# Kernel optimization log

Hardware: AMD Instinct MI355X
Metric: run time of the kernel (lower is better)

Reference implementation:

```python
import jax, jax.numpy as jnp
import numpy as np

NUM_HEADS = 16

def _rope_tables(seq_len, dim, dtype):
    # LongLlamaRotaryEmbedding: inv_freq = 1/10000^(2i/d), emb = cat(freqs, freqs)
    inv_freq = 1.0 / (10000.0 ** (jnp.arange(0, dim, 2, dtype=jnp.float32) / dim))
    t = jnp.arange(seq_len, dtype=jnp.float32)
    freqs = t[:, None] * inv_freq[None, :]            # [S, D/2]
    emb = jnp.concatenate([freqs, freqs], axis=-1)    # [S, D]
    return jnp.cos(emb).astype(dtype), jnp.sin(emb).astype(dtype)

def _rotate_half(x):
    x1, x2 = jnp.split(x, 2, axis=-1)
    return jnp.concatenate([-x2, x1], axis=-1)

def _rotate_one(x, cos, sin, pos):
    # x: [B,H,S,D]; pos: [B,S] int -> gather-indexed RoPE
    c = cos[pos][:, None, :, :]  # [B,1,S,D]
    s = sin[pos][:, None, :, :]
    return x * c + _rotate_half(x) * s

def setup_inputs() -> dict:
    key = jax.random.key(0)
    B, S, HID = 1, 4096, 2048
    ks = jax.random.split(key, 5)
    hidden_states = jax.random.normal(ks[0], (B, S, HID), dtype=jnp.float32)
    # causal additive mask [B,1,S,S]: 0 where allowed, large negative above diagonal
    causal = jnp.tril(jnp.ones((S, S), dtype=bool))
    attention_mask = jnp.where(causal, 0.0, -1e9).astype(jnp.float32)[None, None]
    attention_mask = jnp.broadcast_to(attention_mask, (B, 1, S, S))
    position_ids = jnp.broadcast_to(jnp.arange(S, dtype=jnp.int64), (B, S))
    scale = 0.02
    Wq = jax.random.normal(ks[1], (HID, HID), dtype=jnp.float32) * scale
    Wk = jax.random.normal(ks[2], (HID, HID), dtype=jnp.float32) * scale
    Wv = jax.random.normal(ks[3], (HID, HID), dtype=jnp.float32) * scale
    Wo = jax.random.normal(ks[4], (HID, HID), dtype=jnp.float32) * scale
    return {"hidden_states": hidden_states, "attention_mask": attention_mask,
            "position_ids": position_ids, "Wq": Wq, "Wk": Wk, "Wv": Wv, "Wo": Wo}

def reference(hidden_states, attention_mask, position_ids, Wq, Wk, Wv, Wo):
    B, S, HID = hidden_states.shape
    H = NUM_HEADS
    D = HID // H
    # QKV projections (torch Linear: y = x @ W.T), shaped [B,H,S,D]
    q = (hidden_states @ Wq.T).reshape(B, S, H, D).transpose(0, 2, 1, 3)
    k = (hidden_states @ Wk.T).reshape(B, S, H, D).transpose(0, 2, 1, 3)
    v = (hidden_states @ Wv.T).reshape(B, S, H, D).transpose(0, 2, 1, 3)
    kv_seq_len = k.shape[-2]
    cos, sin = _rope_tables(kv_seq_len, D, hidden_states.dtype)
    # rel_pos_ids = position_ids - min over seq (gather-indexed RoPE)
    rel = position_ids - jnp.min(position_ids, axis=-1, keepdims=True)
    q = _rotate_one(q, cos, sin, rel[:, -S:])
    k = _rotate_one(k, cos, sin, rel)
    scores = jnp.einsum('bhqd,bhkd->bhqk', q, k) / jnp.asarray(np.sqrt(D), hidden_states.dtype)
    scores = scores + attention_mask  # additive mask broadcast over heads
    attn = jax.nn.softmax(scores, axis=-1)
    out = jnp.einsum('bhqk,bhkd->bhqd', attn, v)
    out = out.transpose(0, 2, 1, 3).reshape(B, S, HID)
    return out @ Wo.T
```

## Files before the change

kernel.cpp:

```cpp
#include <hip/hip_runtime.h>
#include <stdint.h>

typedef uint16_t u16;
typedef __bf16 bf16x8 __attribute__((ext_vector_type(8)));
typedef float f32x4 __attribute__((ext_vector_type(4)));
typedef uint32_t u32x4 __attribute__((ext_vector_type(4)));

__device__ __forceinline__ u16 f2bf(float f) {
    uint32_t u = __builtin_bit_cast(uint32_t, f);
    u += 0x7fffu + ((u >> 16) & 1u);
    return (u16)(u >> 16);
}
__device__ __forceinline__ float bf2f(u16 h) {
    uint32_t u = ((uint32_t)h) << 16;
    return __builtin_bit_cast(float, u);
}

__global__ __launch_bounds__(256) void cvt_f32_bf16(const float* __restrict__ in,
                                                    u16* __restrict__ out, int n4) {
    int i = blockIdx.x * 256 + threadIdx.x;
    if (i >= n4) return;
    float4 v = ((const float4*)in)[i];
    u16 o[4] = { f2bf(v.x), f2bf(v.y), f2bf(v.z), f2bf(v.w) };
    *(uint64_t*)(out + 4 * (size_t)i) = *(const uint64_t*)o;
}

__device__ __forceinline__ void gload16(const u16* g, u16* l) {
    __builtin_amdgcn_global_load_lds(
        (const __attribute__((address_space(1))) void*)g,
        (__attribute__((address_space(3))) void*)l, 16, 0, 0);
}

template <int OMODE>
__global__ __launch_bounds__(256) void gemm_bt(const u16* __restrict__ A,
                                               const u16* __restrict__ B,
                                               void* __restrict__ C0,
                                               void* __restrict__ C1,
                                               void* __restrict__ C2,
                                               int M, int N, int K) {
    __shared__ u16 As[128 * 32];
    __shared__ u16 Bs[128 * 32];
    const int tid  = threadIdx.x;
    const int wave = tid >> 6, lane = tid & 63;
    const int quad = lane >> 4, ln = lane & 15;
    const int bm = blockIdx.x, bn = blockIdx.y;
    const int wm = (wave & 1) * 64, wn = (wave >> 1) * 64;
    const u16* Ab = A + (size_t)bm * 128 * K;
    const u16* Bb = B + (size_t)bn * 128 * K;
    const int r0 = tid >> 2, g0 = (tid & 3) * 8;
    const int r1 = 64 + r0;
    u16* AsW0 = As + wave * 512;
    u16* AsW1 = As + 2048 + wave * 512;
    u16* BsW0 = Bs + wave * 512;
    u16* BsW1 = Bs + 2048 + wave * 512;

    f32x4 acc[4][4] = {};
    for (int k0 = 0; k0 < K; k0 += 32) {
        gload16(Ab + (size_t)r0 * K + k0 + g0, AsW0);
        gload16(Ab + (size_t)r1 * K + k0 + g0, AsW1);
        gload16(Bb + (size_t)r0 * K + k0 + g0, BsW0);
        gload16(Bb + (size_t)r1 * K + k0 + g0, BsW1);
        __syncthreads();
        bf16x8 a[4], b[4];
#pragma unroll
        for (int i = 0; i < 4; i++) {
            a[i] = *(const bf16x8*)(As + (wm + i * 16 + ln) * 32 + quad * 8);
            b[i] = *(const bf16x8*)(Bs + (wn + i * 16 + ln) * 32 + quad * 8);
        }
#pragma unroll
        for (int i = 0; i < 4; i++)
#pragma unroll
            for (int j = 0; j < 4; j++)
                acc[i][j] = __builtin_amdgcn_mfma_f32_16x16x32_bf16(a[i], b[j], acc[i][j], 0, 0, 0);
        __syncthreads();
    }
    u16* outB = nullptr;
    if (OMODE == 1) outB = (u16*)(bn < 16 ? C0 : (bn < 32 ? C1 : C2));
#pragma unroll
    for (int i = 0; i < 4; i++)
#pragma unroll
        for (int j = 0; j < 4; j++)
#pragma unroll
            for (int r = 0; r < 4; r++) {
                size_t row = (size_t)(bm * 128 + wm + i * 16 + quad * 4 + r);
                float v = acc[i][j][r];
                if (OMODE == 0) {
                    size_t col = (size_t)(bn * 128 + wn + j * 16 + ln);
                    ((float*)C0)[row * N + col] = v;
                } else {
                    int coll = (bn & 15) * 128 + wn + j * 16 + ln;
                    outB[row * 2048 + coll] = f2bf(v);
                }
            }
}

__global__ __launch_bounds__(256) void rope_scale(u16* __restrict__ Qb,
                                                  u16* __restrict__ Kb) {
    int idx = blockIdx.x * 256 + threadIdx.x;
    int s   = idx >> 11;
    int rem = idx & 2047;
    int mat = rem >> 10;
    int h   = (rem >> 6) & 15;
    int j   = rem & 63;
    u16* base = (mat ? Kb : Qb) + (size_t)s * 2048 + h * 128;
    float x1 = bf2f(base[j]);
    float x2 = bf2f(base[j + 64]);
    float invf = exp2f((float)(-j) * 0.2076205059304601f);
    float th = (float)s * invf;
    float sn, cs;
    sincosf(th, &sn, &cs);
    float o1 = x1 * cs - x2 * sn;
    float o2 = x2 * cs + x1 * sn;
    const float QS = 0.08838834764831845f * 1.4426950408889634f;
    if (mat == 0) { o1 *= QS; o2 *= QS; }
    base[j]      = f2bf(o1);
    base[j + 64] = f2bf(o2);
}

__global__ __launch_bounds__(256) void transpose_v(const u16* __restrict__ V,
                                                   u16* __restrict__ Vt) {
    const int h  = blockIdx.y;
    const int s0 = blockIdx.x * 64;
    const int tid = threadIdx.x;
    for (int c = tid; c < 1024; c += 256) {
        int d = c >> 3, sc = c & 7;
        u16 tmp[8];
#pragma unroll
        for (int j = 0; j < 8; j++)
            tmp[j] = V[(size_t)(s0 + sc * 8 + j) * 2048 + h * 128 + d];
        *(u32x4*)(Vt + ((size_t)h * 128 + d) * 4096 + s0 + sc * 8) = *(const u32x4*)tmp;
    }
}

__global__ __launch_bounds__(256, 3) void fattn(const u16* __restrict__ Qb,
                                                const u16* __restrict__ Kb,
                                                const u16* __restrict__ Vt,
                                                u16* __restrict__ Out) {
    __shared__ u16 Ks[2][32 * 128];
    __shared__ u16 Vs[2][128 * 32];
    __shared__ u16 Ps[128][40];
    const int tid  = threadIdx.x, wave = tid >> 6, lane = tid & 63;
    const int quad = lane >> 4, ln = lane & 15;
    const int h  = blockIdx.y;
    const int qt = 31 - blockIdx.x;
    const int q0 = qt * 128;

    const u16* Kp0 = Kb + h * 128;
    const u16* Vp0 = Vt + (size_t)h * 128 * 4096;

    bf16x8 aq[2][4];
    const u16* Qp = Qb + (size_t)q0 * 2048 + h * 128;
#pragma unroll
    for (int i = 0; i < 2; i++)
#pragma unroll
        for (int ks = 0; ks < 4; ks++)
            aq[i][ks] = *(const bf16x8*)(Qp + (size_t)(wave * 32 + i * 16 + ln) * 2048
                                         + ks * 32 + quad * 8);

    f32x4 o[2][8] = {};
    float lreg[2][4] = {};
    const int nkt = 4 * qt + 4;

    auto stage = [&](int kt, int b) {
        const u16* Kp = Kp0 + (size_t)(kt * 32) * 2048;
        const u16* Vp = Vp0 + kt * 32;
#pragma unroll
        for (int t = 0; t < 2; t++) {
            int p = (wave * 2 + t) * 64 + lane;
            int r = p >> 4, jc = (p & 15) ^ (r & 15);
            gload16(Kp + (size_t)r * 2048 + jc * 8, &Ks[b][(wave * 2 + t) * 512]);
        }
#pragma unroll
        for (int t = 0; t < 2; t++) {
            int p = (wave * 2 + t) * 64 + lane;
            int r = p >> 2, jc = (p & 3) ^ (r & 3);
            gload16(Vp + (size_t)r * 4096 + jc * 8, &Vs[b][(wave * 2 + t) * 512]);
        }
    };

    stage(0, 0);
    for (int kt = 0; kt < nkt; kt++) {
        __syncthreads();
        if (kt + 1 < nkt) stage(kt + 1, (kt + 1) & 1);
        const u16* Ksb = Ks[kt & 1];
        const u16* Vsb = Vs[kt & 1];

        f32x4 sc[2][2] = {};
#pragma unroll
        for (int ks = 0; ks < 4; ks++) {
#pragma unroll
            for (int j = 0; j < 2; j++) {
                int r = j * 16 + ln;
                bf16x8 bk = *(const bf16x8*)(Ksb + (size_t)(r * 16 + ((ks * 4 + quad) ^ ln)) * 8);
                sc[0][j] = __builtin_amdgcn_mfma_f32_16x16x32_bf16(aq[0][ks], bk, sc[0][j], 0, 0, 0);
                sc[1][j] = __builtin_amdgcn_mfma_f32_16x16x32_bf16(aq[1][ks], bk, sc[1][j], 0, 0, 0);
            }
        }
        const int kv0 = kt * 32;
        if (kv0 + 31 > q0 + wave * 32) {
#pragma unroll
            for (int j = 0; j < 2; j++) {
                int col = kv0 + j * 16 + ln;
#pragma unroll
                for (int i = 0; i < 2; i++)
#pragma unroll
                    for (int r = 0; r < 4; r++) {
                        int row = q0 + wave * 32 + i * 16 + quad * 4 + r;
                        if (col > row) sc[i][j][r] = -1e30f;
                    }
            }
        }
#pragma unroll
        for (int i = 0; i < 2; i++) {
#pragma unroll
            for (int r = 0; r < 4; r++) {
                float p0 = __builtin_amdgcn_exp2f(sc[i][0][r]);
                float p1 = __builtin_amdgcn_exp2f(sc[i][1][r]);
                lreg[i][r] += p0 + p1;
                int row = wave * 32 + i * 16 + quad * 4 + r;
                Ps[row][ln]      = f2bf(p0);
                Ps[row][16 + ln] = f2bf(p1);
            }
        }
        bf16x8 pa0 = *(const bf16x8*)&Ps[wave * 32 + ln][quad * 8];
        bf16x8 pa1 = *(const bf16x8*)&Ps[wave * 32 + 16 + ln][quad * 8];
#pragma unroll
        for (int n = 0; n < 8; n++) {
            int rv = n * 16 + ln;
            bf16x8 vb = *(const bf16x8*)(Vsb + (size_t)(rv * 4 + (quad ^ (ln & 3))) * 8);
            o[0][n] = __builtin_amdgcn_mfma_f32_16x16x32_bf16(pa0, vb, o[0][n], 0, 0, 0);
            o[1][n] = __builtin_amdgcn_mfma_f32_16x16x32_bf16(pa1, vb, o[1][n], 0, 0, 0);
        }
    }
    u16* Op = Out + (size_t)(q0 + wave * 32) * 2048 + h * 128;
#pragma unroll
    for (int i = 0; i < 2; i++)
#pragma unroll
        for (int r = 0; r < 4; r++) {
            float l = lreg[i][r];
            l += __shfl_xor(l, 1);
            l += __shfl_xor(l, 2);
            l += __shfl_xor(l, 4);
            l += __shfl_xor(l, 8);
            float inv = 1.0f / l;
            size_t rowoff = (size_t)(i * 16 + quad * 4 + r) * 2048;
#pragma unroll
            for (int n = 0; n < 8; n++)
                Op[rowoff + n * 16 + ln] = f2bf(o[i][n][r] * inv);
        }
}

extern "C" void kernel_launch(void* const* d_in, const int* in_sizes, int n_in,
                              void* d_out, int out_size, void* d_ws, size_t ws_size,
                              hipStream_t stream) {
    const float* hs = (const float*)d_in[0];
    const float* Wq = (const float*)d_in[3];
    const float* Wk = (const float*)d_in[4];
    const float* Wv = (const float*)d_in[5];
    const float* Wo = (const float*)d_in[6];

    char* ws = (char*)d_ws;
    u16* Xb   = (u16*)ws;
    u16* Wob  = (u16*)(ws + (size_t)16777216);
    u16* Qb   = (u16*)(ws + (size_t)25165824);
    u16* Kb   = (u16*)(ws + (size_t)41943040);
    u16* Vtg  = (u16*)(ws + (size_t)58720256);
    u16* Wqkv = (u16*)(ws + (size_t)75497472);
    u16* Vb   = (u16*)(ws + (size_t)100663296);
    u16* attn = Xb;

    cvt_f32_bf16<<<8192, 256, 0, stream>>>(hs, Xb, 2097152);
    cvt_f32_bf16<<<4096, 256, 0, stream>>>(Wq, Wqkv,            1048576);
    cvt_f32_bf16<<<4096, 256, 0, stream>>>(Wk, Wqkv + 4194304,  1048576);
    cvt_f32_bf16<<<4096, 256, 0, stream>>>(Wv, Wqkv + 8388608,  1048576);
    cvt_f32_bf16<<<4096, 256, 0, stream>>>(Wo, Wob,             1048576);

    gemm_bt<1><<<dim3(32, 48), 256, 0, stream>>>(Xb, Wqkv, Qb, Kb, Vb, 4096, 6144, 2048);
    rope_scale<<<32768, 256, 0, stream>>>(Qb, Kb);
    transpose_v<<<dim3(64, 16), 256, 0, stream>>>(Vb, Vtg);
    fattn<<<dim3(32, 16), 256, 0, stream>>>(Qb, Kb, Vtg, attn);
    gemm_bt<0><<<dim3(32, 16), 256, 0, stream>>>(attn, Wob, (float*)d_out, nullptr, nullptr,
                                                 4096, 2048, 2048);
}
```

Measured before the change: 574.2 us.

## Drop LDS staging in attention, trim per-wave causal work, add 64-row output GEMM

The attention kernel stops staging K/V tiles in shared memory with a double buffer and instead has each wave load K and V fragments straight from global memory. Each wave now loops only up to its own causal limit, and the mask is applied only on its last tile. The grid is reordered so heads vary fastest, which may improve L2 reuse of K/V. The output projection switches to a new 64x128-tile GEMM without prefetch, giving more blocks at the cost of less reuse. Direct global loads add latency and redundant traffic across waves, and waves within a block finish unevenly.

Measured after the change: 722.1 us. +25.8%, slower.

```diff
diff --git a/kernel.cpp b/kernel.cpp
--- a/kernel.cpp
+++ b/kernel.cpp
@@ -94,6 +94,57 @@
             }
 }
 
+__global__ __launch_bounds__(256) void gemm_bt64(const u16* __restrict__ A,
+                                                 const u16* __restrict__ B,
+                                                 float* __restrict__ C,
+                                                 int M, int N, int K) {
+    __shared__ u16 As[64 * 32];
+    __shared__ u16 Bs[128 * 32];
+    const int tid  = threadIdx.x;
+    const int wave = tid >> 6, lane = tid & 63;
+    const int quad = lane >> 4, ln = lane & 15;
+    const int bm = blockIdx.x, bn = blockIdx.y;
+    const int wm = (wave & 1) * 32, wn = (wave >> 1) * 64;
+    const u16* Ab = A + (size_t)bm * 64 * K;
+    const u16* Bb = B + (size_t)bn * 128 * K;
+    const int pa = wave * 64 + lane, ra = pa >> 2, ga = (pa & 3) * 8;
+
+    f32x4 acc[2][4] = {};
+    for (int k0 = 0; k0 < K; k0 += 32) {
+        gload16(Ab + (size_t)ra * K + k0 + ga, As + wave * 512);
+#pragma unroll
+        for (int t = 0; t < 2; t++) {
+            int p = (wave * 2 + t) * 64 + lane;
+            int r = p >> 2, g = (p & 3) * 8;
+            gload16(Bb + (size_t)r * K + k0 + g, Bs + (wave * 2 + t) * 512);
+        }
+        __syncthreads();
+        bf16x8 a[2], b[4];
+#pragma unroll
+        for (int i = 0; i < 2; i++)
+            a[i] = *(const bf16x8*)(As + (wm + i * 16 + ln) * 32 + quad * 8);
+#pragma unroll
+        for (int j = 0; j < 4; j++)
+            b[j] = *(const bf16x8*)(Bs + (wn + j * 16 + ln) * 32 + quad * 8);
+#pragma unroll
+        for (int i = 0; i < 2; i++)
+#pragma unroll
+            for (int j = 0; j < 4; j++)
+                acc[i][j] = __builtin_amdgcn_mfma_f32_16x16x32_bf16(a[i], b[j], acc[i][j], 0, 0, 0);
+        __syncthreads();
+    }
+#pragma unroll
+    for (int i = 0; i < 2; i++)
+#pragma unroll
+        for (int j = 0; j < 4; j++)
+#pragma unroll
+            for (int r = 0; r < 4; r++) {
+                size_t row = (size_t)(bm * 64 + wm + i * 16 + quad * 4 + r);
+                size_t col = (size_t)(bn * 128 + wn + j * 16 + ln);
+                C[row * N + col] = acc[i][j][r];
+            }
+}
+
 __global__ __launch_bounds__(256) void rope_scale(u16* __restrict__ Qb,
                                                   u16* __restrict__ Kb) {
     int idx = blockIdx.x * 256 + threadIdx.x;
@@ -136,13 +187,11 @@
                                                 const u16* __restrict__ Kb,
                                                 const u16* __restrict__ Vt,
                                                 u16* __restrict__ Out) {
-    __shared__ u16 Ks[2][32 * 128];
-    __shared__ u16 Vs[2][128 * 32];
     __shared__ u16 Ps[128][40];
     const int tid  = threadIdx.x, wave = tid >> 6, lane = tid & 63;
     const int quad = lane >> 4, ln = lane & 15;
-    const int h  = blockIdx.y;
-    const int qt = 31 - blockIdx.x;
+    const int h  = blockIdx.x;
+    const int qt = 31 - blockIdx.y;
     const int q0 = qt * 128;
 
     const u16* Kp0 = Kb + h * 128;
@@ -159,45 +208,27 @@
 
     f32x4 o[2][8] = {};
     float lreg[2][4] = {};
-    const int nkt = 4 * qt + 4;
-
-    auto stage = [&](int kt, int b) {
-        const u16* Kp = Kp0 + (size_t)(kt * 32) * 2048;
-        const u16* Vp = Vp0 + kt * 32;
-#pragma unroll
-        for (int t = 0; t < 2; t++) {
-            int p = (wave * 2 + t) * 64 + lane;
-            int r = p >> 4, jc = (p & 15) ^ (r & 15);
-            gload16(Kp + (size_t)r * 2048 + jc * 8, &Ks[b][(wave * 2 + t) * 512]);
-        }
-#pragma unroll
-        for (int t = 0; t < 2; t++) {
-            int p = (wave * 2 + t) * 64 + lane;
-            int r = p >> 2, jc = (p & 3) ^ (r & 3);
-            gload16(Vp + (size_t)r * 4096 + jc * 8, &Vs[b][(wave * 2 + t) * 512]);
-        }
-    };
-
-    stage(0, 0);
-    for (int kt = 0; kt < nkt; kt++) {
-        __syncthreads();
-        if (kt + 1 < nkt) stage(kt + 1, (kt + 1) & 1);
-        const u16* Ksb = Ks[kt & 1];
-        const u16* Vsb = Vs[kt & 1];
-
+    const int nktw = 4 * qt + wave + 1;
+
+    for (int kt = 0; kt < nktw; kt++) {
+        const int kv0 = kt * 32;
+        const u16* Kp = Kp0 + (size_t)kv0 * 2048;
+        bf16x8 bk[2][4];
+#pragma unroll
+        for (int j = 0; j < 2; j++)
+#pragma unroll
+            for (int ks = 0; ks < 4; ks++)
+                bk[j][ks] = *(const bf16x8*)(Kp + (size_t)(j * 16 + ln) * 2048
+                                             + ks * 32 + quad * 8);
         f32x4 sc[2][2] = {};
 #pragma unroll
-        for (int ks = 0; ks < 4; ks++) {
+        for (int ks = 0; ks < 4; ks++)
 #pragma unroll
             for (int j = 0; j < 2; j++) {
-                int r = j * 16 + ln;
-                bf16x8 bk = *(const bf16x8*)(Ksb + (size_t)(r * 16 + ((ks * 4 + quad) ^ ln)) * 8);
-                sc[0][j] = __builtin_amdgcn_mfma_f32_16x16x32_bf16(aq[0][ks], bk, sc[0][j], 0, 0, 0);
-                sc[1][j] = __builtin_amdgcn_mfma_f32_16x16x32_bf16(aq[1][ks], bk, sc[1][j], 0, 0, 0);
-            }
-        }
-        const int kv0 = kt * 32;
-        if (kv0 + 31 > q0 + wave * 32) {
+                sc[0][j] = __builtin_amdgcn_mfma_f32_16x16x32_bf16(aq[0][ks], bk[j][ks], sc[0][j], 0, 0, 0);
+                sc[1][j] = __builtin_amdgcn_mfma_f32_16x16x32_bf16(aq[1][ks], bk[j][ks], sc[1][j], 0, 0, 0);
+            }
+        if (kt == nktw - 1) {
 #pragma unroll
             for (int j = 0; j < 2; j++) {
                 int col = kv0 + j * 16 + ln;
@@ -211,7 +242,7 @@
             }
         }
 #pragma unroll
-        for (int i = 0; i < 2; i++) {
+        for (int i = 0; i < 2; i++)
 #pragma unroll
             for (int r = 0; r < 4; r++) {
                 float p0 = __builtin_amdgcn_exp2f(sc[i][0][r]);
@@ -221,13 +252,12 @@
                 Ps[row][ln]      = f2bf(p0);
                 Ps[row][16 + ln] = f2bf(p1);
             }
-        }
         bf16x8 pa0 = *(const bf16x8*)&Ps[wave * 32 + ln][quad * 8];
         bf16x8 pa1 = *(const bf16x8*)&Ps[wave * 32 + 16 + ln][quad * 8];
+        const u16* Vp = Vp0 + kv0;
 #pragma unroll
         for (int n = 0; n < 8; n++) {
-            int rv = n * 16 + ln;
-            bf16x8 vb = *(const bf16x8*)(Vsb + (size_t)(rv * 4 + (quad ^ (ln & 3))) * 8);
+            bf16x8 vb = *(const bf16x8*)(Vp + (size_t)(n * 16 + ln) * 4096 + quad * 8);
             o[0][n] = __builtin_amdgcn_mfma_f32_16x16x32_bf16(pa0, vb, o[0][n], 0, 0, 0);
             o[1][n] = __builtin_amdgcn_mfma_f32_16x16x32_bf16(pa1, vb, o[1][n], 0, 0, 0);
         }
@@ -278,7 +308,6 @@
     gemm_bt<1><<<dim3(32, 48), 256, 0, stream>>>(Xb, Wqkv, Qb, Kb, Vb, 4096, 6144, 2048);
     rope_scale<<<32768, 256, 0, stream>>>(Qb, Kb);
     transpose_v<<<dim3(64, 16), 256, 0, stream>>>(Vb, Vtg);
-    fattn<<<dim3(32, 16), 256, 0, stream>>>(Qb, Kb, Vtg, attn);
-    gemm_bt<0><<<dim3(32, 16), 256, 0, stream>>>(attn, Wob, (float*)d_out, nullptr, nullptr,
-                                                 4096, 2048, 2048);
-}
+    fattn<<<dim3(16, 32), 256, 0, stream>>>(Qb, Kb, Vtg, attn);
+    gemm_bt64<<<dim3(64, 16), 256, 0, stream>>>(attn, Wob, (float*)d_out, 4096, 2048, 2048);
+}
```
